# Kernel tuning notes

Measured on AMD Instinct MI355X. Metric: run time of the kernel, lower is better.

Reference implementation:

```python
import jax, jax.numpy as jnp
import numpy as np

DT = 0.01
NJ = 7  # panda: 7 revolute joints, serial chain, fixed base
G_ACC = 9.81


def skew(v):
    x, y, z = v[..., 0], v[..., 1], v[..., 2]
    O = jnp.zeros_like(x)
    return jnp.stack([jnp.stack([O, -z, y], -1),
                      jnp.stack([z, O, -x], -1),
                      jnp.stack([-y, x, O], -1)], -2)


def rodrigues(axis, q):
    # axis [3], q [B] -> [B,3,3]
    K = skew(axis)
    K2 = K @ K
    s = jnp.sin(q)[:, None, None]
    c = jnp.cos(q)[:, None, None]
    return jnp.eye(3, dtype=q.dtype) + s * K + (1.0 - c) * K2


def xmot(E, r, v):
    # motion transform child<-parent; E [B,3,3], r [3], v [B,6] ([w;u] ordering)
    w, u = v[:, :3], v[:, 3:]
    wn = jnp.einsum('bij,bj->bi', E, w)
    un = jnp.einsum('bij,bj->bi', E, u - jnp.cross(jnp.broadcast_to(r, u.shape), w))
    return jnp.concatenate([wn, un], -1)


def crm(v, m):
    # motion cross product v x m
    w, u = v[:, :3], v[:, 3:]
    return jnp.concatenate([jnp.cross(w, m[:, :3]),
                            jnp.cross(w, m[:, 3:]) + jnp.cross(u, m[:, :3])], -1)


def crf(v, f):
    # force cross product v x* f
    w, u = v[:, :3], v[:, 3:]
    n, ff = f[:, :3], f[:, 3:]
    return jnp.concatenate([jnp.cross(w, n) + jnp.cross(u, ff), jnp.cross(w, ff)], -1)


def spatial_inertia(mass, com, inertia):
    # [NJ] / [NJ,3] / [NJ,3,3] -> [NJ,6,6] in [w;v] ordering
    cx = skew(com)
    m = mass[:, None, None]
    top = jnp.concatenate([inertia + m * (cx @ jnp.swapaxes(cx, -1, -2)), m * cx], -1)
    bot = jnp.concatenate([m * jnp.swapaxes(cx, -1, -2),
                           m * jnp.broadcast_to(jnp.eye(3, dtype=mass.dtype), cx.shape)], -1)
    return jnp.concatenate([top, bot], -2)


def aba(q, qd, tau, axes, R_fix, p_fix, mass, com, inertia):
    B = q.shape[0]
    I6 = spatial_inertia(mass, com, inertia)  # [NJ,6,6]
    E_l, S_l, v_l, c_l, IA_l, pA_l = [], [], [], [], [], []
    v_prev = None
    # pass 1: kinematics + bias terms
    for i in range(NJ):
        Rw = jnp.einsum('ij,bjk->bik', R_fix[i], rodrigues(axes[i], q[:, i]))
        E = jnp.swapaxes(Rw, -1, -2)  # parent->child rotation
        S = jnp.concatenate([axes[i], jnp.zeros(3, dtype=q.dtype)])  # [6]
        vJ = qd[:, i:i + 1] * S
        v_i = vJ if i == 0 else xmot(E, p_fix[i], v_prev) + vJ
        c_i = crm(v_i, vJ)
        Iv = jnp.einsum('ij,bj->bi', I6[i], v_i)
        pA_i = crf(v_i, Iv)
        E_l.append(E); S_l.append(S); v_l.append(v_i); c_l.append(c_i)
        IA_l.append(jnp.broadcast_to(I6[i], (B, 6, 6)))
        pA_l.append(pA_i)
        v_prev = v_i
    # pass 2: articulated inertia backward sweep
    U_l = [None] * NJ; d_l = [None] * NJ; uu_l = [None] * NJ
    for i in reversed(range(NJ)):
        S = S_l[i]; IA = IA_l[i]
        U = jnp.einsum('bij,j->bi', IA, S)
        d = jnp.einsum('bi,i->b', U, S)
        uu = tau[:, i] - jnp.einsum('bi,i->b', pA_l[i], S)
        U_l[i], d_l[i], uu_l[i] = U, d, uu
        if i > 0:
            Ia = IA - U[:, :, None] * U[:, None, :] / d[:, None, None]
            pa = pA_l[i] + jnp.einsum('bij,bj->bi', Ia, c_l[i]) + U * (uu / d)[:, None]
            E = E_l[i]; rX = skew(p_fix[i])
            Z = jnp.zeros_like(E)
            Xm = jnp.concatenate([jnp.concatenate([E, Z], -1),
                                  jnp.concatenate([-jnp.einsum('bij,jk->bik', E, rX), E], -1)], -2)
            IA_l[i - 1] = IA_l[i - 1] + jnp.einsum('bji,bjk,bkl->bil', Xm, Ia, Xm)
            fE = jnp.einsum('bji,bj->bi', E, pa[:, 3:])
            nP = jnp.einsum('bji,bj->bi', E, pa[:, :3]) + jnp.cross(jnp.broadcast_to(p_fix[i], fE.shape), fE)
            pA_l[i - 1] = pA_l[i - 1] + jnp.concatenate([nP, fE], -1)
    # pass 3: accelerations (base spatial accel = -gravity)
    a_prev = jnp.broadcast_to(jnp.array([0, 0, 0, 0, 0, G_ACC], dtype=q.dtype), (B, 6))
    qdd = []
    for i in range(NJ):
        ap = xmot(E_l[i], p_fix[i], a_prev) + c_l[i]
        qdd_i = (uu_l[i] - jnp.einsum('bi,bi->b', U_l[i], ap)) / d_l[i]
        a_prev = ap + qdd_i[:, None] * S_l[i]
        qdd.append(qdd_i)
    return jnp.stack(qdd, -1)  # [B,NJ]


def _rx(a):
    c, s = np.cos(a), np.sin(a)
    return np.array([[1, 0, 0], [0, c, -s], [0, s, c]], np.float32)


def setup_inputs() -> dict:
    key = jax.random.key(0)
    k1, k2 = jax.random.split(key)
    B = 262144
    x = 0.5 * jax.random.normal(k1, (B, 2 * NJ), dtype=jnp.float32)
    u = 5.0 * jax.random.normal(k2, (B, NJ), dtype=jnp.float32)
    angles = [0.0, -np.pi / 2, np.pi / 2, np.pi / 2, -np.pi / 2, np.pi / 2, np.pi / 2]
    R_fix = jnp.asarray(np.stack([_rx(a) for a in angles]).astype(np.float32))
    p_fix = jnp.asarray(np.array([[0, 0, 0.333], [0, 0, 0], [0, -0.316, 0], [0.0825, 0, 0],
                                  [-0.0825, 0.384, 0], [0, 0, 0], [0.088, 0, 0]], np.float32))
    axes = jnp.asarray(np.tile(np.array([0, 0, 1], np.float32), (NJ, 1)))
    mass = jnp.asarray(np.array([4.97, 0.65, 3.23, 3.59, 1.23, 1.67, 0.735], np.float32))
    com = jnp.asarray(np.array([[0.003, 0.002, -0.06], [-0.003, -0.028, 0.003], [0.027, 0.039, -0.066],
                                [-0.053, 0.104, 0.027], [-0.012, 0.041, -0.038], [0.06, -0.014, -0.011],
                                [0.01, -0.004, 0.061]], np.float32))
    diags = np.array([[0.7, 0.7, 0.01], [0.008, 0.028, 0.025], [0.037, 0.036, 0.011],
                      [0.026, 0.028, 0.031], [0.036, 0.036, 0.011], [0.002, 0.004, 0.005],
                      [0.012, 0.010, 0.005]], np.float32)
    inertia = jnp.asarray(np.stack([np.diag(v) for v in diags]).astype(np.float32))
    return {"x": x, "u": u, "axes": axes, "R_fix": R_fix, "p_fix": p_fix,
            "mass": mass, "com": com, "inertia": inertia}


def reference(x, u, axes, R_fix, p_fix, mass, com, inertia):
    q, v = x[:, :NJ], x[:, NJ:]
    a = aba(q, v, u, axes, R_fix, p_fix, mass, com, inertia)
    v_next = v + DT * a            # semi-implicit Euler
    q_next = q + DT * v_next
    return jnp.concatenate([q_next, v_next], -1)
```

## Files before the change

kernel.cpp:

```cpp
#include <hip/hip_runtime.h>

#define NJ 7
#define TB 256
static constexpr float DT_C    = 0.01f;
static constexpr float G_ACC_C = 9.81f;

static constexpr float RF[NJ][9] = {
    {1,0,0,  0,1,0,  0,0,1},
    {1,0,0,  0,0,1,  0,-1,0},
    {1,0,0,  0,0,-1, 0,1,0},
    {1,0,0,  0,0,-1, 0,1,0},
    {1,0,0,  0,0,1,  0,-1,0},
    {1,0,0,  0,0,-1, 0,1,0},
    {1,0,0,  0,0,-1, 0,1,0},
};
static constexpr float PFX[NJ][3] = {
    {0.f, 0.f, 0.333f},
    {0.f, 0.f, 0.f},
    {0.f, -0.316f, 0.f},
    {0.0825f, 0.f, 0.f},
    {-0.0825f, 0.384f, 0.f},
    {0.f, 0.f, 0.f},
    {0.088f, 0.f, 0.f},
};
static constexpr float MS[NJ] = {4.97f, 0.65f, 3.23f, 3.59f, 1.23f, 1.67f, 0.735f};
static constexpr float CM[NJ][3] = {
    {0.003f, 0.002f, -0.06f},
    {-0.003f, -0.028f, 0.003f},
    {0.027f, 0.039f, -0.066f},
    {-0.053f, 0.104f, 0.027f},
    {-0.012f, 0.041f, -0.038f},
    {0.06f, -0.014f, -0.011f},
    {0.01f, -0.004f, 0.061f},
};
static constexpr float ID[NJ][3] = {
    {0.7f, 0.7f, 0.01f},
    {0.008f, 0.028f, 0.025f},
    {0.037f, 0.036f, 0.011f},
    {0.026f, 0.028f, 0.031f},
    {0.036f, 0.036f, 0.011f},
    {0.002f, 0.004f, 0.005f},
    {0.012f, 0.01f, 0.005f},
};

struct Derived {
    float J[NJ][6];
    float MC[NJ][3];
};
static constexpr Derived make_derived() {
    Derived d{};
    for (int i = 0; i < NJ; ++i) {
        float m = MS[i], cx = CM[i][0], cy = CM[i][1], cz = CM[i][2];
        float cc = cx*cx + cy*cy + cz*cz;
        d.J[i][0] = ID[i][0] + m*(cc - cx*cx);
        d.J[i][1] = -(m*cx*cy);
        d.J[i][2] = -(m*cx*cz);
        d.J[i][3] = ID[i][1] + m*(cc - cy*cy);
        d.J[i][4] = -(m*cy*cz);
        d.J[i][5] = ID[i][2] + m*(cc - cz*cz);
        d.MC[i][0] = m*cx; d.MC[i][1] = m*cy; d.MC[i][2] = m*cz;
    }
    return d;
}
static constexpr Derived DRV = make_derived();

#define MAKE_E(Rf, s, c)                                                     \
    float E00 = (Rf)[0]*(c) + (Rf)[1]*(s);                                   \
    float E01 = (Rf)[3]*(c) + (Rf)[4]*(s);                                   \
    float E02 = (Rf)[6]*(c) + (Rf)[7]*(s);                                   \
    float E10 = (Rf)[1]*(c) - (Rf)[0]*(s);                                   \
    float E11 = (Rf)[4]*(c) - (Rf)[3]*(s);                                   \
    float E12 = (Rf)[7]*(c) - (Rf)[6]*(s);                                   \
    float E20 = (Rf)[2];                                                     \
    float E21 = (Rf)[5];                                                     \
    float E22 = (Rf)[8];

extern "C" __global__ __launch_bounds__(TB)
void aba_step_kernel(const float* __restrict__ x, const float* __restrict__ u,
                     float* __restrict__ out, int B)
{
    __shared__ float vbuf[TB * 37];

    const int tid = threadIdx.x;
    const int b   = blockIdx.x * TB + tid;
    if (b >= B) return;
    const int xb = b * 14;
    float* vr = vbuf + tid * 37;

    float qr[NJ], qdr[NJ];
    #pragma unroll
    for (int i = 0; i < NJ; ++i) qr[i]  = x[xb + i];
    #pragma unroll
    for (int i = 0; i < NJ; ++i) qdr[i] = x[xb + 7 + i];

    float v0, v1, v2, v3, v4, v5;

    {
        v0 = 0.f; v1 = 0.f; v2 = qdr[0]; v3 = 0.f; v4 = 0.f; v5 = 0.f;
        vr[0] = v0; vr[1] = v1; vr[2] = v2; vr[3] = v3; vr[4] = v4; vr[5] = v5;
        #pragma unroll
        for (int i = 1; i < NJ; ++i) {
            float s, c;
            __sincosf(qr[i], &s, &c);
            MAKE_E(RF[i], s, c)
            const float px = PFX[i][0], py = PFX[i][1], pz = PFX[i][2];
            float t0 = v3 - (py*v2 - pz*v1);
            float t1 = v4 - (pz*v0 - px*v2);
            float t2 = v5 - (px*v1 - py*v0);
            float nw0 = E00*v0 + E01*v1 + E02*v2;
            float nw1 = E10*v0 + E11*v1 + E12*v2;
            float nw2 = E20*v0 + E21*v1 + E22*v2;
            float nu0 = E00*t0 + E01*t1 + E02*t2;
            float nu1 = E10*t0 + E11*t1 + E12*t2;
            float nu2 = E20*t0 + E21*t1 + E22*t2;
            v0 = nw0; v1 = nw1; v2 = nw2 + qdr[i];
            v3 = nu0; v4 = nu1; v5 = nu2;
            if (i < 6) {
                vr[6*i+0] = v0; vr[6*i+1] = v1; vr[6*i+2] = v2;
                vr[6*i+3] = v3; vr[6*i+4] = v4; vr[6*i+5] = v5;
            }
        }
    }

    float PA[6] = {0,0,0,0,0,0};
    float PB[9] = {0,0,0,0,0,0,0,0,0};
    float PC[6] = {0,0,0,0,0,0};
    float AC0=0.f, AC1=0.f, AC2=0.f, AC3=0.f, AC4=0.f, AC5=0.f;
    float u60=0.f, u61=0.f, u62=0.f, u63=0.f, u64=0.f, u65=0.f;

    #pragma unroll 1
    for (int i = 6; i >= 1; --i) {
        const float qd = x[xb + 7 + i];
        const float m   = MS[i];
        const float mcx = DRV.MC[i][0], mcy = DRV.MC[i][1], mcz = DRV.MC[i][2];
        const float J0 = DRV.J[i][0], J1 = DRV.J[i][1], J2 = DRV.J[i][2];
        const float J3 = DRV.J[i][3], J4 = DRV.J[i][4], J5 = DRV.J[i][5];

        float n0 = J0*v0 + J1*v1 + J2*v2 + (mcy*v5 - mcz*v4);
        float n1 = J1*v0 + J3*v1 + J4*v2 + (mcz*v3 - mcx*v5);
        float n2 = J2*v0 + J4*v1 + J5*v2 + (mcx*v4 - mcy*v3);
        float f0 = v1*mcz - v2*mcy + m*v3;
        float f1 = v2*mcx - v0*mcz + m*v4;
        float f2 = v0*mcy - v1*mcx + m*v5;
        float p0 = v1*n2 - v2*n1 + v4*f2 - v5*f1 + AC0;
        float p1 = v2*n0 - v0*n2 + v5*f0 - v3*f2 + AC1;
        float p2 = v0*n1 - v1*n0 + v3*f1 - v4*f0 + AC2;
        float p3 = v1*f2 - v2*f1 + AC3;
        float p4 = v2*f0 - v0*f2 + AC4;
        float p5 = v0*f1 - v1*f0 + AC5;

        float A0 = J0 + PA[0]; float A1 = J1 + PA[1]; float A2 = J2 + PA[2];
        float A3 = J3 + PA[3]; float A4 = J4 + PA[4]; float A5 = J5 + PA[5];
        float B00 = PB[0];        float B01 = PB[1] - mcz;  float B02 = PB[2] + mcy;
        float B10 = PB[3] + mcz;  float B11 = PB[4];        float B12 = PB[5] - mcx;
        float B20 = PB[6] - mcy;  float B21 = PB[7] + mcx;  float B22 = PB[8];
        float C0 = PC[0] + m, C1 = PC[1],     C2 = PC[2];
        float C3 = PC[3] + m, C4 = PC[4],     C5 = PC[5] + m;

        float uu   = u[b*NJ + i] - p2;
        float invd = __builtin_amdgcn_rcpf(A5);
        float k    = uu * invd;
        float t0 = A2*invd, t1 = A4*invd;
        float t3 = B20*invd, t4 = B21*invd, t5 = B22*invd;

        if (i == 6) {
            u60 = t0; u61 = t1; u62 = t3; u63 = t4; u64 = t5; u65 = k;
        } else {
            vr[6*i+0] = t0; vr[6*i+1] = t1; vr[6*i+2] = t3;
            vr[6*i+3] = t4; vr[6*i+4] = t5; vr[6*i+5] = k;
        }

        float a00 = A0 - A2*t0, a01 = A1 - A2*t1, a11 = A3 - A4*t1;
        float b00 = B00 - A2*t3, b01 = B01 - A2*t4, b02 = B02 - A2*t5;
        float b10 = B10 - A4*t3, b11 = B11 - A4*t4, b12 = B12 - A4*t5;
        float c00 = C0 - B20*t3, c01 = C1 - B20*t4, c02 = C2 - B20*t5;
        float c11 = C3 - B21*t4, c12 = C4 - B21*t5, c22 = C5 - B22*t5;

        float q0 = v1*qd, q1 = -v0*qd, q3 = v4*qd, q4 = -v3*qd;
        float pa0 = p0 + a00*q0 + a01*q1 + b00*q3 + b01*q4 + A2*k;
        float pa1 = p1 + a01*q0 + a11*q1 + b10*q3 + b11*q4 + A4*k;
        float pa2 = p2 + uu;
        float pa3 = p3 + b00*q0 + b10*q1 + c00*q3 + c01*q4 + B20*k;
        float pa4 = p4 + b01*q0 + b11*q1 + c01*q3 + c11*q4 + B21*k;
        float pa5 = p5 + b02*q0 + b12*q1 + c02*q3 + c12*q4 + B22*k;

        float s, c;
        __sincosf(x[xb + i], &s, &c);
        const float R0 = RF[i][0], R1 = RF[i][1], R3 = RF[i][3],
                    R4 = RF[i][4], R6 = RF[i][6], R7 = RF[i][7];
        float E00 = R0*c + R1*s, E01 = R3*c + R4*s, E02 = R6*c + R7*s;
        float E10 = R1*c - R0*s, E11 = R4*c - R3*s, E12 = R7*c - R6*s;
        const float E20 = RF[i][2], E21 = RF[i][5], E22 = RF[i][8];
        const float px = PFX[i][0], py = PFX[i][1], pz = PFX[i][2];

        float fE0 = E00*pa3 + E10*pa4 + E20*pa5;
        float fE1 = E01*pa3 + E11*pa4 + E21*pa5;
        float fE2 = E02*pa3 + E12*pa4 + E22*pa5;
        AC0 = E00*pa0 + E10*pa1 + E20*pa2 + (py*fE2 - pz*fE1);
        AC1 = E01*pa0 + E11*pa1 + E21*pa2 + (pz*fE0 - px*fE2);
        AC2 = E02*pa0 + E12*pa1 + E22*pa2 + (px*fE1 - py*fE0);
        AC3 = fE0; AC4 = fE1; AC5 = fE2;

        float AE00 = a00*E00 + a01*E10, AE01 = a00*E01 + a01*E11, AE02 = a00*E02 + a01*E12;
        float AE10 = a01*E00 + a11*E10, AE11 = a01*E01 + a11*E11, AE12 = a01*E02 + a11*E12;
        float Ap00 = E00*AE00 + E10*AE10;
        float Ap01 = E00*AE01 + E10*AE11;
        float Ap02 = E00*AE02 + E10*AE12;
        float Ap11 = E01*AE01 + E11*AE11;
        float Ap12 = E01*AE02 + E11*AE12;
        float Ap22 = E02*AE02 + E12*AE12;
        float BE00 = b00*E00 + b01*E10 + b02*E20;
        float BE01 = b00*E01 + b01*E11 + b02*E21;
        float BE02 = b00*E02 + b01*E12 + b02*E22;
        float BE10 = b10*E00 + b11*E10 + b12*E20;
        float BE11 = b10*E01 + b11*E11 + b12*E21;
        float BE12 = b10*E02 + b11*E12 + b12*E22;
        float Bp00 = E00*BE00 + E10*BE10, Bp01 = E00*BE01 + E10*BE11, Bp02 = E00*BE02 + E10*BE12;
        float Bp10 = E01*BE00 + E11*BE10, Bp11 = E01*BE01 + E11*BE11, Bp12 = E01*BE02 + E11*BE12;
        float Bp20 = E02*BE00 + E12*BE10, Bp21 = E02*BE01 + E12*BE11, Bp22 = E02*BE02 + E12*BE12;
        float CE00 = c00*E00 + c01*E10 + c02*E20;
        float CE01 = c00*E01 + c01*E11 + c02*E21;
        float CE02 = c00*E02 + c01*E12 + c02*E22;
        float CE10 = c01*E00 + c11*E10 + c12*E20;
        float CE11 = c01*E01 + c11*E11 + c12*E21;
        float CE12 = c01*E02 + c11*E12 + c12*E22;
        float CE20 = c02*E00 + c12*E10 + c22*E20;
        float CE21 = c02*E01 + c12*E11 + c22*E21;
        float CE22 = c02*E02 + c12*E12 + c22*E22;
        float Cp00 = E00*CE00 + E10*CE10 + E20*CE20;
        float Cp01 = E00*CE01 + E10*CE11 + E20*CE21;
        float Cp02 = E00*CE02 + E10*CE12 + E20*CE22;
        float Cp11 = E01*CE01 + E11*CE11 + E21*CE21;
        float Cp12 = E01*CE02 + E11*CE12 + E21*CE22;
        float Cp22 = E02*CE02 + E12*CE12 + E22*CE22;
        float G00 = Bp01*pz - Bp02*py, G01 = Bp02*px - Bp00*pz, G02 = Bp00*py - Bp01*px;
        float G10 = Bp11*pz - Bp12*py, G11 = Bp12*px - Bp10*pz, G12 = Bp10*py - Bp11*px;
        float G20 = Bp21*pz - Bp22*py, G21 = Bp22*px - Bp20*pz, G22 = Bp20*py - Bp21*px;
        float H00 = Cp01*pz - Cp02*py, H01 = Cp02*px - Cp00*pz, H02 = Cp00*py - Cp01*px;
        float H10 = Cp11*pz - Cp12*py, H11 = Cp12*px - Cp01*pz, H12 = Cp01*py - Cp11*px;
        float H20 = Cp12*pz - Cp22*py, H21 = Cp22*px - Cp02*pz, H22 = Cp02*py - Cp12*px;
        float PH00 = py*H20 - pz*H10;
        float PH01 = py*H21 - pz*H11;
        float PH02 = py*H22 - pz*H12;
        float PH11 = pz*H01 - px*H21;
        float PH12 = pz*H02 - px*H22;
        float PH22 = px*H12 - py*H02;

        float nv0 = vr[6*(i-1)+0], nv1 = vr[6*(i-1)+1], nv2 = vr[6*(i-1)+2];
        float nv3 = vr[6*(i-1)+3], nv4 = vr[6*(i-1)+4], nv5 = vr[6*(i-1)+5];

        PA[0] = Ap00 - G00 - G00 - PH00;
        PA[1] = Ap01 - G01 - G10 - PH01;
        PA[2] = Ap02 - G02 - G20 - PH02;
        PA[3] = Ap11 - G11 - G11 - PH11;
        PA[4] = Ap12 - G12 - G21 - PH12;
        PA[5] = Ap22 - G22 - G22 - PH22;
        PB[0] = Bp00 + py*Cp02 - pz*Cp01;
        PB[1] = Bp01 + py*Cp12 - pz*Cp11;
        PB[2] = Bp02 + py*Cp22 - pz*Cp12;
        PB[3] = Bp10 + pz*Cp00 - px*Cp02;
        PB[4] = Bp11 + pz*Cp01 - px*Cp12;
        PB[5] = Bp12 + pz*Cp02 - px*Cp22;
        PB[6] = Bp20 + px*Cp01 - py*Cp00;
        PB[7] = Bp21 + px*Cp11 - py*Cp01;
        PB[8] = Bp22 + px*Cp12 - py*Cp02;
        PC[0] = Cp00; PC[1] = Cp01; PC[2] = Cp02;
        PC[3] = Cp11; PC[4] = Cp12; PC[5] = Cp22;

        v0 = nv0; v1 = nv1; v2 = nv2; v3 = nv3; v4 = nv4; v5 = nv5;
    }

    {
        const float m   = MS[0];
        const float mcx = DRV.MC[0][0], mcy = DRV.MC[0][1], mcz = DRV.MC[0][2];
        const float J0 = DRV.J[0][0], J1 = DRV.J[0][1], J2 = DRV.J[0][2];
        const float J3 = DRV.J[0][3], J4 = DRV.J[0][4], J5 = DRV.J[0][5];
        float n0 = J0*v0 + J1*v1 + J2*v2 + (mcy*v5 - mcz*v4);
        float n1 = J1*v0 + J3*v1 + J4*v2 + (mcz*v3 - mcx*v5);
        float n2 = J2*v0 + J4*v1 + J5*v2 + (mcx*v4 - mcy*v3);
        float f0 = v1*mcz - v2*mcy + m*v3;
        float f1 = v2*mcx - v0*mcz + m*v4;
        float f2 = v0*mcy - v1*mcx + m*v5;
        float p2 = v0*n1 - v1*n0 + v3*f1 - v4*f0 + AC2;
        float A2 = J2 + PA[2];
        float A4 = J4 + PA[4];
        float A5 = J5 + PA[5];
        float B20 = PB[6] - mcy;  float B21 = PB[7] + mcx;  float B22 = PB[8];
        float uu   = u[b*NJ + 0] - p2;
        float invd = __builtin_amdgcn_rcpf(A5);
        float k    = uu * invd;
        vr[0] = A2*invd; vr[1] = A4*invd; vr[2] = B20*invd;
        vr[3] = B21*invd; vr[4] = B22*invd; vr[5] = k;
        (void)n2; (void)f2;
    }

    {
        float a0=0.f, a1=0.f, a2=0.f, a3=0.f, a4=0.f, a5=G_ACC_C;
        float w0=0.f, w1=0.f, w2=0.f, w3=0.f, w4=0.f, w5=0.f;
        #pragma unroll
        for (int i = 0; i < NJ; ++i) {
            const float qd = qdr[i];
            float s, c;
            __sincosf(qr[i], &s, &c);
            MAKE_E(RF[i], s, c)
            const float px = PFX[i][0], py = PFX[i][1], pz = PFX[i][2];
            if (i == 0) {
                w2 = qd;
            } else {
                float r0 = w3 - (py*w2 - pz*w1);
                float r1 = w4 - (pz*w0 - px*w2);
                float r2 = w5 - (px*w1 - py*w0);
                float nw0 = E00*w0 + E01*w1 + E02*w2;
                float nw1 = E10*w0 + E11*w1 + E12*w2;
                float nw2 = E20*w0 + E21*w1 + E22*w2;
                float nu0 = E00*r0 + E01*r1 + E02*r2;
                float nu1 = E10*r0 + E11*r1 + E12*r2;
                float nu2 = E20*r0 + E21*r1 + E22*r2;
                w0 = nw0; w1 = nw1; w2 = nw2 + qd;
                w3 = nu0; w4 = nu1; w5 = nu2;
            }
            float cl0 = w1*qd, cl1 = -w0*qd, cl3 = w4*qd, cl4 = -w3*qd;
            float r0 = a3 - (py*a2 - pz*a1);
            float r1 = a4 - (pz*a0 - px*a2);
            float r2 = a5 - (px*a1 - py*a0);
            float ap0 = E00*a0 + E01*a1 + E02*a2 + cl0;
            float ap1 = E10*a0 + E11*a1 + E12*a2 + cl1;
            float ap2 = E20*a0 + E21*a1 + E22*a2;
            float ap3 = E00*r0 + E01*r1 + E02*r2 + cl3;
            float ap4 = E10*r0 + E11*r1 + E12*r2 + cl4;
            float ap5 = E20*r0 + E21*r1 + E22*r2;
            float d0, d1, d2, d3, d4, d5;
            if (i == 6) {
                d0 = u60; d1 = u61; d2 = u62; d3 = u63; d4 = u64; d5 = u65;
            } else {
                d0 = vr[6*i+0]; d1 = vr[6*i+1]; d2 = vr[6*i+2];
                d3 = vr[6*i+3]; d4 = vr[6*i+4]; d5 = vr[6*i+5];
            }
            float qdd = d5 - (d0*ap0 + d1*ap1 + ap2 + d2*ap3 + d3*ap4 + d4*ap5);
            a0 = ap0; a1 = ap1; a2 = ap2 + qdd;
            a3 = ap3; a4 = ap4; a5 = ap5;
            float vn = qd + DT_C*qdd;
            out[xb + 7 + i] = vn;
            out[xb + i]     = qr[i] + DT_C*vn;
        }
    }
}

extern "C" void kernel_launch(void* const* d_in, const int* in_sizes, int n_in,
                              void* d_out, int out_size, void* d_ws, size_t ws_size,
                              hipStream_t stream) {
    const float* x = (const float*)d_in[0];
    const float* u = (const float*)d_in[1];
    float* out = (float*)d_out;
    int B = in_sizes[0] / (2*NJ);
    int threads = TB;
    int blocks = (B + threads - 1) / threads;
    hipLaunchKernelGGL(aba_step_kernel, dim3(blocks), dim3(threads), 0, stream,
                       x, u, out, B);
}
```

Before: 108.1 us.

## Process two batch elements per thread with interleaved independent dependency chains

Each thread now handles two robots, sample t and sample t+B/2, and the forward, backward and final passes interleave the work of both. The goal is more instruction-level parallelism, so the long serial ABA dependency chains can hide each other's latency. The block size is halved to keep shared memory per block the same. In exchange, register pressure roughly doubles, which may cut occupancy or cause spills. Joint angles and rates are now reloaded from global memory instead of being cached in registers.

Result: slower. 118.2 us (+9.3%).

```diff
diff --git a/kernel.cpp b/kernel.cpp
--- a/kernel.cpp
+++ b/kernel.cpp
@@ -1,7 +1,7 @@
 #include <hip/hip_runtime.h>
 
 #define NJ 7
-#define TB 256
+#define TB 128
 static constexpr float DT_C    = 0.01f;
 static constexpr float G_ACC_C = 9.81f;
 
@@ -79,31 +79,39 @@
 void aba_step_kernel(const float* __restrict__ x, const float* __restrict__ u,
                      float* __restrict__ out, int B)
 {
-    __shared__ float vbuf[TB * 37];
-
-    const int tid = threadIdx.x;
-    const int b   = blockIdx.x * TB + tid;
-    if (b >= B) return;
-    const int xb = b * 14;
-    float* vr = vbuf + tid * 37;
-
-    float qr[NJ], qdr[NJ];
+    __shared__ float vbuf[2 * TB * 37];
+
+    const int tid    = threadIdx.x;
+    const int halfUp = (B + 1) >> 1;
+    const int t      = blockIdx.x * TB + tid;
+    if (t >= halfUp) return;
+    int b1 = t + halfUp;
+    if (b1 >= B) b1 = t;
+    const int bb[2] = { t, b1 };
+    const int xb[2] = { bb[0] * 14, bb[1] * 14 };
+    float* const vr[2] = { vbuf + tid * 37, vbuf + (TB + tid) * 37 };
+
+    float v[2][6];
+
     #pragma unroll
-    for (int i = 0; i < NJ; ++i) qr[i]  = x[xb + i];
+    for (int it = 0; it < 2; ++it) {
+        float qd0 = x[xb[it] + 7];
+        v[it][0]=0.f; v[it][1]=0.f; v[it][2]=qd0;
+        v[it][3]=0.f; v[it][4]=0.f; v[it][5]=0.f;
+        vr[it][0]=0.f; vr[it][1]=0.f; vr[it][2]=qd0;
+        vr[it][3]=0.f; vr[it][4]=0.f; vr[it][5]=0.f;
+    }
     #pragma unroll
-    for (int i = 0; i < NJ; ++i) qdr[i] = x[xb + 7 + i];
-
-    float v0, v1, v2, v3, v4, v5;
-
-    {
-        v0 = 0.f; v1 = 0.f; v2 = qdr[0]; v3 = 0.f; v4 = 0.f; v5 = 0.f;
-        vr[0] = v0; vr[1] = v1; vr[2] = v2; vr[3] = v3; vr[4] = v4; vr[5] = v5;
+    for (int i = 1; i < NJ; ++i) {
         #pragma unroll
-        for (int i = 1; i < NJ; ++i) {
+        for (int it = 0; it < 2; ++it) {
             float s, c;
-            __sincosf(qr[i], &s, &c);
+            __sincosf(x[xb[it] + i], &s, &c);
             MAKE_E(RF[i], s, c)
             const float px = PFX[i][0], py = PFX[i][1], pz = PFX[i][2];
+            const float qd = x[xb[it] + 7 + i];
+            float v0=v[it][0], v1=v[it][1], v2=v[it][2];
+            float v3=v[it][3], v4=v[it][4], v5=v[it][5];
             float t0 = v3 - (py*v2 - pz*v1);
             float t1 = v4 - (pz*v0 - px*v2);
             float t2 = v5 - (px*v1 - py*v0);
@@ -113,235 +121,263 @@
             float nu0 = E00*t0 + E01*t1 + E02*t2;
             float nu1 = E10*t0 + E11*t1 + E12*t2;
             float nu2 = E20*t0 + E21*t1 + E22*t2;
-            v0 = nw0; v1 = nw1; v2 = nw2 + qdr[i];
-            v3 = nu0; v4 = nu1; v5 = nu2;
+            v[it][0]=nw0; v[it][1]=nw1; v[it][2]=nw2+qd;
+            v[it][3]=nu0; v[it][4]=nu1; v[it][5]=nu2;
             if (i < 6) {
-                vr[6*i+0] = v0; vr[6*i+1] = v1; vr[6*i+2] = v2;
-                vr[6*i+3] = v3; vr[6*i+4] = v4; vr[6*i+5] = v5;
+                vr[it][6*i+0]=v[it][0]; vr[it][6*i+1]=v[it][1]; vr[it][6*i+2]=v[it][2];
+                vr[it][6*i+3]=v[it][3]; vr[it][6*i+4]=v[it][4]; vr[it][6*i+5]=v[it][5];
             }
         }
     }
 
-    float PA[6] = {0,0,0,0,0,0};
-    float PB[9] = {0,0,0,0,0,0,0,0,0};
-    float PC[6] = {0,0,0,0,0,0};
-    float AC0=0.f, AC1=0.f, AC2=0.f, AC3=0.f, AC4=0.f, AC5=0.f;
-    float u60=0.f, u61=0.f, u62=0.f, u63=0.f, u64=0.f, u65=0.f;
+    float PAa[2][6] = {{0,0,0,0,0,0},{0,0,0,0,0,0}};
+    float PBa[2][9] = {{0,0,0,0,0,0,0,0,0},{0,0,0,0,0,0,0,0,0}};
+    float PCa[2][6] = {{0,0,0,0,0,0},{0,0,0,0,0,0}};
+    float ACa[2][6] = {{0,0,0,0,0,0},{0,0,0,0,0,0}};
+    float U6[2][6];
 
     #pragma unroll 1
     for (int i = 6; i >= 1; --i) {
-        const float qd = x[xb + 7 + i];
         const float m   = MS[i];
         const float mcx = DRV.MC[i][0], mcy = DRV.MC[i][1], mcz = DRV.MC[i][2];
         const float J0 = DRV.J[i][0], J1 = DRV.J[i][1], J2 = DRV.J[i][2];
         const float J3 = DRV.J[i][3], J4 = DRV.J[i][4], J5 = DRV.J[i][5];
-
-        float n0 = J0*v0 + J1*v1 + J2*v2 + (mcy*v5 - mcz*v4);
-        float n1 = J1*v0 + J3*v1 + J4*v2 + (mcz*v3 - mcx*v5);
-        float n2 = J2*v0 + J4*v1 + J5*v2 + (mcx*v4 - mcy*v3);
-        float f0 = v1*mcz - v2*mcy + m*v3;
-        float f1 = v2*mcx - v0*mcz + m*v4;
-        float f2 = v0*mcy - v1*mcx + m*v5;
-        float p0 = v1*n2 - v2*n1 + v4*f2 - v5*f1 + AC0;
-        float p1 = v2*n0 - v0*n2 + v5*f0 - v3*f2 + AC1;
-        float p2 = v0*n1 - v1*n0 + v3*f1 - v4*f0 + AC2;
-        float p3 = v1*f2 - v2*f1 + AC3;
-        float p4 = v2*f0 - v0*f2 + AC4;
-        float p5 = v0*f1 - v1*f0 + AC5;
-
-        float A0 = J0 + PA[0]; float A1 = J1 + PA[1]; float A2 = J2 + PA[2];
-        float A3 = J3 + PA[3]; float A4 = J4 + PA[4]; float A5 = J5 + PA[5];
-        float B00 = PB[0];        float B01 = PB[1] - mcz;  float B02 = PB[2] + mcy;
-        float B10 = PB[3] + mcz;  float B11 = PB[4];        float B12 = PB[5] - mcx;
-        float B20 = PB[6] - mcy;  float B21 = PB[7] + mcx;  float B22 = PB[8];
-        float C0 = PC[0] + m, C1 = PC[1],     C2 = PC[2];
-        float C3 = PC[3] + m, C4 = PC[4],     C5 = PC[5] + m;
-
-        float uu   = u[b*NJ + i] - p2;
-        float invd = __builtin_amdgcn_rcpf(A5);
-        float k    = uu * invd;
-        float t0 = A2*invd, t1 = A4*invd;
-        float t3 = B20*invd, t4 = B21*invd, t5 = B22*invd;
-
-        if (i == 6) {
-            u60 = t0; u61 = t1; u62 = t3; u63 = t4; u64 = t5; u65 = k;
-        } else {
-            vr[6*i+0] = t0; vr[6*i+1] = t1; vr[6*i+2] = t3;
-            vr[6*i+3] = t4; vr[6*i+4] = t5; vr[6*i+5] = k;
-        }
-
-        float a00 = A0 - A2*t0, a01 = A1 - A2*t1, a11 = A3 - A4*t1;
-        float b00 = B00 - A2*t3, b01 = B01 - A2*t4, b02 = B02 - A2*t5;
-        float b10 = B10 - A4*t3, b11 = B11 - A4*t4, b12 = B12 - A4*t5;
-        float c00 = C0 - B20*t3, c01 = C1 - B20*t4, c02 = C2 - B20*t5;
-        float c11 = C3 - B21*t4, c12 = C4 - B21*t5, c22 = C5 - B22*t5;
-
-        float q0 = v1*qd, q1 = -v0*qd, q3 = v4*qd, q4 = -v3*qd;
-        float pa0 = p0 + a00*q0 + a01*q1 + b00*q3 + b01*q4 + A2*k;
-        float pa1 = p1 + a01*q0 + a11*q1 + b10*q3 + b11*q4 + A4*k;
-        float pa2 = p2 + uu;
-        float pa3 = p3 + b00*q0 + b10*q1 + c00*q3 + c01*q4 + B20*k;
-        float pa4 = p4 + b01*q0 + b11*q1 + c01*q3 + c11*q4 + B21*k;
-        float pa5 = p5 + b02*q0 + b12*q1 + c02*q3 + c12*q4 + B22*k;
-
-        float s, c;
-        __sincosf(x[xb + i], &s, &c);
         const float R0 = RF[i][0], R1 = RF[i][1], R3 = RF[i][3],
                     R4 = RF[i][4], R6 = RF[i][6], R7 = RF[i][7];
-        float E00 = R0*c + R1*s, E01 = R3*c + R4*s, E02 = R6*c + R7*s;
-        float E10 = R1*c - R0*s, E11 = R4*c - R3*s, E12 = R7*c - R6*s;
-        const float E20 = RF[i][2], E21 = RF[i][5], E22 = RF[i][8];
+        const float E20c = RF[i][2], E21c = RF[i][5], E22c = RF[i][8];
         const float px = PFX[i][0], py = PFX[i][1], pz = PFX[i][2];
 
-        float fE0 = E00*pa3 + E10*pa4 + E20*pa5;
-        float fE1 = E01*pa3 + E11*pa4 + E21*pa5;
-        float fE2 = E02*pa3 + E12*pa4 + E22*pa5;
-        AC0 = E00*pa0 + E10*pa1 + E20*pa2 + (py*fE2 - pz*fE1);
-        AC1 = E01*pa0 + E11*pa1 + E21*pa2 + (pz*fE0 - px*fE2);
-        AC2 = E02*pa0 + E12*pa1 + E22*pa2 + (px*fE1 - py*fE0);
-        AC3 = fE0; AC4 = fE1; AC5 = fE2;
-
-        float AE00 = a00*E00 + a01*E10, AE01 = a00*E01 + a01*E11, AE02 = a00*E02 + a01*E12;
-        float AE10 = a01*E00 + a11*E10, AE11 = a01*E01 + a11*E11, AE12 = a01*E02 + a11*E12;
-        float Ap00 = E00*AE00 + E10*AE10;
-        float Ap01 = E00*AE01 + E10*AE11;
-        float Ap02 = E00*AE02 + E10*AE12;
-        float Ap11 = E01*AE01 + E11*AE11;
-        float Ap12 = E01*AE02 + E11*AE12;
-        float Ap22 = E02*AE02 + E12*AE12;
-        float BE00 = b00*E00 + b01*E10 + b02*E20;
-        float BE01 = b00*E01 + b01*E11 + b02*E21;
-        float BE02 = b00*E02 + b01*E12 + b02*E22;
-        float BE10 = b10*E00 + b11*E10 + b12*E20;
-        float BE11 = b10*E01 + b11*E11 + b12*E21;
-        float BE12 = b10*E02 + b11*E12 + b12*E22;
-        float Bp00 = E00*BE00 + E10*BE10, Bp01 = E00*BE01 + E10*BE11, Bp02 = E00*BE02 + E10*BE12;
-        float Bp10 = E01*BE00 + E11*BE10, Bp11 = E01*BE01 + E11*BE11, Bp12 = E01*BE02 + E11*BE12;
-        float Bp20 = E02*BE00 + E12*BE10, Bp21 = E02*BE01 + E12*BE11, Bp22 = E02*BE02 + E12*BE12;
-        float CE00 = c00*E00 + c01*E10 + c02*E20;
-        float CE01 = c00*E01 + c01*E11 + c02*E21;
-        float CE02 = c00*E02 + c01*E12 + c02*E22;
-        float CE10 = c01*E00 + c11*E10 + c12*E20;
-        float CE11 = c01*E01 + c11*E11 + c12*E21;
-        float CE12 = c01*E02 + c11*E12 + c12*E22;
-        float CE20 = c02*E00 + c12*E10 + c22*E20;
-        float CE21 = c02*E01 + c12*E11 + c22*E21;
-        float CE22 = c02*E02 + c12*E12 + c22*E22;
-        float Cp00 = E00*CE00 + E10*CE10 + E20*CE20;
-        float Cp01 = E00*CE01 + E10*CE11 + E20*CE21;
-        float Cp02 = E00*CE02 + E10*CE12 + E20*CE22;
-        float Cp11 = E01*CE01 + E11*CE11 + E21*CE21;
-        float Cp12 = E01*CE02 + E11*CE12 + E21*CE22;
-        float Cp22 = E02*CE02 + E12*CE12 + E22*CE22;
-        float G00 = Bp01*pz - Bp02*py, G01 = Bp02*px - Bp00*pz, G02 = Bp00*py - Bp01*px;
-        float G10 = Bp11*pz - Bp12*py, G11 = Bp12*px - Bp10*pz, G12 = Bp10*py - Bp11*px;
-        float G20 = Bp21*pz - Bp22*py, G21 = Bp22*px - Bp20*pz, G22 = Bp20*py - Bp21*px;
-        float H00 = Cp01*pz - Cp02*py, H01 = Cp02*px - Cp00*pz, H02 = Cp00*py - Cp01*px;
-        float H10 = Cp11*pz - Cp12*py, H11 = Cp12*px - Cp01*pz, H12 = Cp01*py - Cp11*px;
-        float H20 = Cp12*pz - Cp22*py, H21 = Cp22*px - Cp02*pz, H22 = Cp02*py - Cp12*px;
-        float PH00 = py*H20 - pz*H10;
-        float PH01 = py*H21 - pz*H11;
-        float PH02 = py*H22 - pz*H12;
-        float PH11 = pz*H01 - px*H21;
-        float PH12 = pz*H02 - px*H22;
-        float PH22 = px*H12 - py*H02;
-
-        float nv0 = vr[6*(i-1)+0], nv1 = vr[6*(i-1)+1], nv2 = vr[6*(i-1)+2];
-        float nv3 = vr[6*(i-1)+3], nv4 = vr[6*(i-1)+4], nv5 = vr[6*(i-1)+5];
-
-        PA[0] = Ap00 - G00 - G00 - PH00;
-        PA[1] = Ap01 - G01 - G10 - PH01;
-        PA[2] = Ap02 - G02 - G20 - PH02;
-        PA[3] = Ap11 - G11 - G11 - PH11;
-        PA[4] = Ap12 - G12 - G21 - PH12;
-        PA[5] = Ap22 - G22 - G22 - PH22;
-        PB[0] = Bp00 + py*Cp02 - pz*Cp01;
-        PB[1] = Bp01 + py*Cp12 - pz*Cp11;
-        PB[2] = Bp02 + py*Cp22 - pz*Cp12;
-        PB[3] = Bp10 + pz*Cp00 - px*Cp02;
-        PB[4] = Bp11 + pz*Cp01 - px*Cp12;
-        PB[5] = Bp12 + pz*Cp02 - px*Cp22;
-        PB[6] = Bp20 + px*Cp01 - py*Cp00;
-        PB[7] = Bp21 + px*Cp11 - py*Cp01;
-        PB[8] = Bp22 + px*Cp12 - py*Cp02;
-        PC[0] = Cp00; PC[1] = Cp01; PC[2] = Cp02;
-        PC[3] = Cp11; PC[4] = Cp12; PC[5] = Cp22;
-
-        v0 = nv0; v1 = nv1; v2 = nv2; v3 = nv3; v4 = nv4; v5 = nv5;
-    }
-
-    {
+        #pragma unroll
+        for (int it = 0; it < 2; ++it) {
+            const float qd  = x[xb[it] + 7 + i];
+            const float tau = u[bb[it]*NJ + i];
+            float s, c;
+            __sincosf(x[xb[it] + i], &s, &c);
+
+            const float v0=v[it][0], v1=v[it][1], v2=v[it][2];
+            const float v3=v[it][3], v4=v[it][4], v5=v[it][5];
+
+            float n0 = J0*v0 + J1*v1 + J2*v2 + (mcy*v5 - mcz*v4);
+            float n1 = J1*v0 + J3*v1 + J4*v2 + (mcz*v3 - mcx*v5);
+            float n2 = J2*v0 + J4*v1 + J5*v2 + (mcx*v4 - mcy*v3);
+            float f0 = v1*mcz - v2*mcy + m*v3;
+            float f1 = v2*mcx - v0*mcz + m*v4;
+            float f2 = v0*mcy - v1*mcx + m*v5;
+            float p0 = v1*n2 - v2*n1 + v4*f2 - v5*f1 + ACa[it][0];
+            float p1 = v2*n0 - v0*n2 + v5*f0 - v3*f2 + ACa[it][1];
+            float p2 = v0*n1 - v1*n0 + v3*f1 - v4*f0 + ACa[it][2];
+            float p3 = v1*f2 - v2*f1 + ACa[it][3];
+            float p4 = v2*f0 - v0*f2 + ACa[it][4];
+            float p5 = v0*f1 - v1*f0 + ACa[it][5];
+
+            float A0 = J0 + PAa[it][0]; float A1 = J1 + PAa[it][1]; float A2 = J2 + PAa[it][2];
+            float A3 = J3 + PAa[it][3]; float A4 = J4 + PAa[it][4]; float A5 = J5 + PAa[it][5];
+            float B00 = PBa[it][0];        float B01 = PBa[it][1] - mcz;  float B02 = PBa[it][2] + mcy;
+            float B10 = PBa[it][3] + mcz;  float B11 = PBa[it][4];        float B12 = PBa[it][5] - mcx;
+            float B20 = PBa[it][6] - mcy;  float B21 = PBa[it][7] + mcx;  float B22 = PBa[it][8];
+            float C0 = PCa[it][0] + m, C1 = PCa[it][1],     C2 = PCa[it][2];
+            float C3 = PCa[it][3] + m, C4 = PCa[it][4],     C5 = PCa[it][5] + m;
+
+            float uu   = tau - p2;
+            float invd = __builtin_amdgcn_rcpf(A5);
+            float k    = uu * invd;
+            float t0 = A2*invd, t1 = A4*invd;
+            float t3 = B20*invd, t4 = B21*invd, t5 = B22*invd;
+
+            if (i == 6) {
+                U6[it][0]=t0; U6[it][1]=t1; U6[it][2]=t3;
+                U6[it][3]=t4; U6[it][4]=t5; U6[it][5]=k;
+            } else {
+                vr[it][6*i+0]=t0; vr[it][6*i+1]=t1; vr[it][6*i+2]=t3;
+                vr[it][6*i+3]=t4; vr[it][6*i+4]=t5; vr[it][6*i+5]=k;
+            }
+
+            float a00 = A0 - A2*t0, a01 = A1 - A2*t1, a11 = A3 - A4*t1;
+            float b00 = B00 - A2*t3, b01 = B01 - A2*t4, b02 = B02 - A2*t5;
+            float b10 = B10 - A4*t3, b11 = B11 - A4*t4, b12 = B12 - A4*t5;
+            float c00 = C0 - B20*t3, c01 = C1 - B20*t4, c02 = C2 - B20*t5;
+            float c11 = C3 - B21*t4, c12 = C4 - B21*t5, c22 = C5 - B22*t5;
+
+            float q0 = v1*qd, q1 = -v0*qd, q3 = v4*qd, q4 = -v3*qd;
+            float pa0 = p0 + a00*q0 + a01*q1 + b00*q3 + b01*q4 + A2*k;
+            float pa1 = p1 + a01*q0 + a11*q1 + b10*q3 + b11*q4 + A4*k;
+            float pa2 = p2 + uu;
+            float pa3 = p3 + b00*q0 + b10*q1 + c00*q3 + c01*q4 + B20*k;
+            float pa4 = p4 + b01*q0 + b11*q1 + c01*q3 + c11*q4 + B21*k;
+            float pa5 = p5 + b02*q0 + b12*q1 + c02*q3 + c12*q4 + B22*k;
+
+            float E00 = R0*c + R1*s, E01 = R3*c + R4*s, E02 = R6*c + R7*s;
+            float E10 = R1*c - R0*s, E11 = R4*c - R3*s, E12 = R7*c - R6*s;
+            const float E20 = E20c, E21 = E21c, E22 = E22c;
+
+            float fE0 = E00*pa3 + E10*pa4 + E20*pa5;
+            float fE1 = E01*pa3 + E11*pa4 + E21*pa5;
+            float fE2 = E02*pa3 + E12*pa4 + E22*pa5;
+            ACa[it][0] = E00*pa0 + E10*pa1 + E20*pa2 + (py*fE2 - pz*fE1);
+            ACa[it][1] = E01*pa0 + E11*pa1 + E21*pa2 + (pz*fE0 - px*fE2);
+            ACa[it][2] = E02*pa0 + E12*pa1 + E22*pa2 + (px*fE1 - py*fE0);
+            ACa[it][3] = fE0; ACa[it][4] = fE1; ACa[it][5] = fE2;
+
+            float AE00 = a00*E00 + a01*E10, AE01 = a00*E01 + a01*E11, AE02 = a00*E02 + a01*E12;
+            float AE10 = a01*E00 + a11*E10, AE11 = a01*E01 + a11*E11, AE12 = a01*E02 + a11*E12;
+            float Ap00 = E00*AE00 + E10*AE10;
+            float Ap01 = E00*AE01 + E10*AE11;
+            float Ap02 = E00*AE02 + E10*AE12;
+            float Ap11 = E01*AE01 + E11*AE11;
+            float Ap12 = E01*AE02 + E11*AE12;
+            float Ap22 = E02*AE02 + E12*AE12;
+            float BE00 = b00*E00 + b01*E10 + b02*E20;
+            float BE01 = b00*E01 + b01*E11 + b02*E21;
+            float BE02 = b00*E02 + b01*E12 + b02*E22;
+            float BE10 = b10*E00 + b11*E10 + b12*E20;
+            float BE11 = b10*E01 + b11*E11 + b12*E21;
+            float BE12 = b10*E02 + b11*E12 + b12*E22;
+            float Bp00 = E00*BE00 + E10*BE10, Bp01 = E00*BE01 + E10*BE11, Bp02 = E00*BE02 + E10*BE12;
+            float Bp10 = E01*BE00 + E11*BE10, Bp11 = E01*BE01 + E11*BE11, Bp12 = E01*BE02 + E11*BE12;
+            float Bp20 = E02*BE00 + E12*BE10, Bp21 = E02*BE01 + E12*BE11, Bp22 = E02*BE02 + E12*BE12;
+            float CE00 = c00*E00 + c01*E10 + c02*E20;
+            float CE01 = c00*E01 + c01*E11 + c02*E21;
+            float CE02 = c00*E02 + c01*E12 + c02*E22;
+            float CE10 = c01*E00 + c11*E10 + c12*E20;
+            float CE11 = c01*E01 + c11*E11 + c12*E21;
+            float CE12 = c01*E02 + c11*E12 + c12*E22;
+            float CE20 = c02*E00 + c12*E10 + c22*E20;
+            float CE21 = c02*E01 + c12*E11 + c22*E21;
+            float CE22 = c02*E02 + c12*E12 + c22*E22;
+            float Cp00 = E00*CE00 + E10*CE10 + E20*CE20;
+            float Cp01 = E00*CE01 + E10*CE11 + E20*CE21;
+            float Cp02 = E00*CE02 + E10*CE12 + E20*CE22;
+            float Cp11 = E01*CE01 + E11*CE11 + E21*CE21;
+            float Cp12 = E01*CE02 + E11*CE12 + E21*CE22;
+            float Cp22 = E02*CE02 + E12*CE12 + E22*CE22;
+            float G00 = Bp01*pz - Bp02*py, G01 = Bp02*px - Bp00*pz, G02 = Bp00*py - Bp01*px;
+            float G10 = Bp11*pz - Bp12*py, G11 = Bp12*px - Bp10*pz, G12 = Bp10*py - Bp11*px;
+            float G20 = Bp21*pz - Bp22*py, G21 = Bp22*px - Bp20*pz, G22 = Bp20*py - Bp21*px;
+            float H00 = Cp01*pz - Cp02*py, H01 = Cp02*px - Cp00*pz, H02 = Cp00*py - Cp01*px;
+            float H10 = Cp11*pz - Cp12*py, H11 = Cp12*px - Cp01*pz, H12 = Cp01*py - Cp11*px;
+            float H20 = Cp12*pz - Cp22*py, H21 = Cp22*px - Cp02*pz, H22 = Cp02*py - Cp12*px;
+            float PH00 = py*H20 - pz*H10;
+            float PH01 = py*H21 - pz*H11;
+            float PH02 = py*H22 - pz*H12;
+            float PH11 = pz*H01 - px*H21;
+            float PH12 = pz*H02 - px*H22;
+            float PH22 = px*H12 - py*H02;
+
+            float nv0 = vr[it][6*(i-1)+0], nv1 = vr[it][6*(i-1)+1], nv2 = vr[it][6*(i-1)+2];
+            float nv3 = vr[it][6*(i-1)+3], nv4 = vr[it][6*(i-1)+4], nv5 = vr[it][6*(i-1)+5];
+
+            PAa[it][0] = Ap00 - G00 - G00 - PH00;
+            PAa[it][1] = Ap01 - G01 - G10 - PH01;
+            PAa[it][2] = Ap02 - G02 - G20 - PH02;
+            PAa[it][3] = Ap11 - G11 - G11 - PH11;
+            PAa[it][4] = Ap12 - G12 - G21 - PH12;
+            PAa[it][5] = Ap22 - G22 - G22 - PH22;
+            PBa[it][0] = Bp00 + py*Cp02 - pz*Cp01;
+            PBa[it][1] = Bp01 + py*Cp12 - pz*Cp11;
+            PBa[it][2] = Bp02 + py*Cp22 - pz*Cp12;
+            PBa[it][3] = Bp10 + pz*Cp00 - px*Cp02;
+            PBa[it][4] = Bp11 + pz*Cp01 - px*Cp12;
+            PBa[it][5] = Bp12 + pz*Cp02 - px*Cp22;
+            PBa[it][6] = Bp20 + px*Cp01 - py*Cp00;
+            PBa[it][7] = Bp21 + px*Cp11 - py*Cp01;
+            PBa[it][8] = Bp22 + px*Cp12 - py*Cp02;
+            PCa[it][0] = Cp00; PCa[it][1] = Cp01; PCa[it][2] = Cp02;
+            PCa[it][3] = Cp11; PCa[it][4] = Cp12; PCa[it][5] = Cp22;
+
+            v[it][0]=nv0; v[it][1]=nv1; v[it][2]=nv2;
+            v[it][3]=nv3; v[it][4]=nv4; v[it][5]=nv5;
+        }
+    }
+
+    #pragma unroll
+    for (int it = 0; it < 2; ++it) {
         const float m   = MS[0];
         const float mcx = DRV.MC[0][0], mcy = DRV.MC[0][1], mcz = DRV.MC[0][2];
         const float J0 = DRV.J[0][0], J1 = DRV.J[0][1], J2 = DRV.J[0][2];
         const float J3 = DRV.J[0][3], J4 = DRV.J[0][4], J5 = DRV.J[0][5];
+        const float v0=v[it][0], v1=v[it][1], v2=v[it][2];
+        const float v3=v[it][3], v4=v[it][4], v5=v[it][5];
         float n0 = J0*v0 + J1*v1 + J2*v2 + (mcy*v5 - mcz*v4);
         float n1 = J1*v0 + J3*v1 + J4*v2 + (mcz*v3 - mcx*v5);
-        float n2 = J2*v0 + J4*v1 + J5*v2 + (mcx*v4 - mcy*v3);
         float f0 = v1*mcz - v2*mcy + m*v3;
         float f1 = v2*mcx - v0*mcz + m*v4;
-        float f2 = v0*mcy - v1*mcx + m*v5;
-        float p2 = v0*n1 - v1*n0 + v3*f1 - v4*f0 + AC2;
-        float A2 = J2 + PA[2];
-        float A4 = J4 + PA[4];
-        float A5 = J5 + PA[5];
-        float B20 = PB[6] - mcy;  float B21 = PB[7] + mcx;  float B22 = PB[8];
-        float uu   = u[b*NJ + 0] - p2;
+        float p2 = v0*n1 - v1*n0 + v3*f1 - v4*f0 + ACa[it][2];
+        float A2 = J2 + PAa[it][2];
+        float A4 = J4 + PAa[it][4];
+        float A5 = J5 + PAa[it][5];
+        float B20 = PBa[it][6] - mcy;  float B21 = PBa[it][7] + mcx;  float B22 = PBa[it][8];
+        float uu   = u[bb[it]*NJ + 0] - p2;
         float invd = __builtin_amdgcn_rcpf(A5);
         float k    = uu * invd;
-        vr[0] = A2*invd; vr[1] = A4*invd; vr[2] = B20*invd;
-        vr[3] = B21*invd; vr[4] = B22*invd; vr[5] = k;
-        (void)n2; (void)f2;
+        vr[it][0] = A2*invd;  vr[it][1] = A4*invd; vr[it][2] = B20*invd;
+        vr[it][3] = B21*invd; vr[it][4] = B22*invd; vr[it][5] = k;
     }
 
     {
-        float a0=0.f, a1=0.f, a2=0.f, a3=0.f, a4=0.f, a5=G_ACC_C;
-        float w0=0.f, w1=0.f, w2=0.f, w3=0.f, w4=0.f, w5=0.f;
+        float aa[2][6], ww[2][6];
+        #pragma unroll
+        for (int it = 0; it < 2; ++it) {
+            aa[it][0]=0.f; aa[it][1]=0.f; aa[it][2]=0.f;
+            aa[it][3]=0.f; aa[it][4]=0.f; aa[it][5]=G_ACC_C;
+            ww[it][0]=0.f; ww[it][1]=0.f; ww[it][2]=0.f;
+            ww[it][3]=0.f; ww[it][4]=0.f; ww[it][5]=0.f;
+        }
         #pragma unroll
         for (int i = 0; i < NJ; ++i) {
-            const float qd = qdr[i];
-            float s, c;
-            __sincosf(qr[i], &s, &c);
-            MAKE_E(RF[i], s, c)
-            const float px = PFX[i][0], py = PFX[i][1], pz = PFX[i][2];
-            if (i == 0) {
-                w2 = qd;
-            } else {
-                float r0 = w3 - (py*w2 - pz*w1);
-                float r1 = w4 - (pz*w0 - px*w2);
-                float r2 = w5 - (px*w1 - py*w0);
-                float nw0 = E00*w0 + E01*w1 + E02*w2;
-                float nw1 = E10*w0 + E11*w1 + E12*w2;
-                float nw2 = E20*w0 + E21*w1 + E22*w2;
-                float nu0 = E00*r0 + E01*r1 + E02*r2;
-                float nu1 = E10*r0 + E11*r1 + E12*r2;
-                float nu2 = E20*r0 + E21*r1 + E22*r2;
-                w0 = nw0; w1 = nw1; w2 = nw2 + qd;
-                w3 = nu0; w4 = nu1; w5 = nu2;
+            #pragma unroll
+            for (int it = 0; it < 2; ++it) {
+                const float qi = x[xb[it] + i];
+                const float qd = x[xb[it] + 7 + i];
+                float s, c;
+                __sincosf(qi, &s, &c);
+                MAKE_E(RF[i], s, c)
+                const float px = PFX[i][0], py = PFX[i][1], pz = PFX[i][2];
+                float w0=ww[it][0], w1=ww[it][1], w2=ww[it][2];
+                float w3=ww[it][3], w4=ww[it][4], w5=ww[it][5];
+                if (i == 0) {
+                    w2 = qd;
+                } else {
+                    float r0 = w3 - (py*w2 - pz*w1);
+                    float r1 = w4 - (pz*w0 - px*w2);
+                    float r2 = w5 - (px*w1 - py*w0);
+                    float nw0 = E00*w0 + E01*w1 + E02*w2;
+                    float nw1 = E10*w0 + E11*w1 + E12*w2;
+                    float nw2 = E20*w0 + E21*w1 + E22*w2;
+                    float nu0 = E00*r0 + E01*r1 + E02*r2;
+                    float nu1 = E10*r0 + E11*r1 + E12*r2;
+                    float nu2 = E20*r0 + E21*r1 + E22*r2;
+                    w0 = nw0; w1 = nw1; w2 = nw2 + qd;
+                    w3 = nu0; w4 = nu1; w5 = nu2;
+                }
+                ww[it][0]=w0; ww[it][1]=w1; ww[it][2]=w2;
+                ww[it][3]=w3; ww[it][4]=w4; ww[it][5]=w5;
+                float cl0 = w1*qd, cl1 = -w0*qd, cl3 = w4*qd, cl4 = -w3*qd;
+                float a0=aa[it][0], a1=aa[it][1], a2=aa[it][2];
+                float a3=aa[it][3], a4=aa[it][4], a5=aa[it][5];
+                float r0 = a3 - (py*a2 - pz*a1);
+                float r1 = a4 - (pz*a0 - px*a2);
+                float r2 = a5 - (px*a1 - py*a0);
+                float ap0 = E00*a0 + E01*a1 + E02*a2 + cl0;
+                float ap1 = E10*a0 + E11*a1 + E12*a2 + cl1;
+                float ap2 = E20*a0 + E21*a1 + E22*a2;
+                float ap3 = E00*r0 + E01*r1 + E02*r2 + cl3;
+                float ap4 = E10*r0 + E11*r1 + E12*r2 + cl4;
+                float ap5 = E20*r0 + E21*r1 + E22*r2;
+                float d0, d1, d2, d3, d4, d5;
+                if (i == 6) {
+                    d0=U6[it][0]; d1=U6[it][1]; d2=U6[it][2];
+                    d3=U6[it][3]; d4=U6[it][4]; d5=U6[it][5];
+                } else {
+                    d0=vr[it][6*i+0]; d1=vr[it][6*i+1]; d2=vr[it][6*i+2];
+                    d3=vr[it][6*i+3]; d4=vr[it][6*i+4]; d5=vr[it][6*i+5];
+                }
+                float qdd = d5 - (d0*ap0 + d1*ap1 + ap2 + d2*ap3 + d3*ap4 + d4*ap5);
+                aa[it][0]=ap0; aa[it][1]=ap1; aa[it][2]=ap2+qdd;
+                aa[it][3]=ap3; aa[it][4]=ap4; aa[it][5]=ap5;
+                float vn = qd + DT_C*qdd;
+                out[xb[it] + 7 + i] = vn;
+                out[xb[it] + i]     = qi + DT_C*vn;
             }
-            float cl0 = w1*qd, cl1 = -w0*qd, cl3 = w4*qd, cl4 = -w3*qd;
-            float r0 = a3 - (py*a2 - pz*a1);
-            float r1 = a4 - (pz*a0 - px*a2);
-            float r2 = a5 - (px*a1 - py*a0);
-            float ap0 = E00*a0 + E01*a1 + E02*a2 + cl0;
-            float ap1 = E10*a0 + E11*a1 + E12*a2 + cl1;
-            float ap2 = E20*a0 + E21*a1 + E22*a2;
-            float ap3 = E00*r0 + E01*r1 + E02*r2 + cl3;
-            float ap4 = E10*r0 + E11*r1 + E12*r2 + cl4;
-            float ap5 = E20*r0 + E21*r1 + E22*r2;
-            float d0, d1, d2, d3, d4, d5;
-            if (i == 6) {
-                d0 = u60; d1 = u61; d2 = u62; d3 = u63; d4 = u64; d5 = u65;
-            } else {
-                d0 = vr[6*i+0]; d1 = vr[6*i+1]; d2 = vr[6*i+2];
-                d3 = vr[6*i+3]; d4 = vr[6*i+4]; d5 = vr[6*i+5];
-            }
-            float qdd = d5 - (d0*ap0 + d1*ap1 + ap2 + d2*ap3 + d3*ap4 + d4*ap5);
-            a0 = ap0; a1 = ap1; a2 = ap2 + qdd;
-            a3 = ap3; a4 = ap4; a5 = ap5;
-            float vn = qd + DT_C*qdd;
-            out[xb + 7 + i] = vn;
-            out[xb + i]     = qr[i] + DT_C*vn;
         }
     }
 }
@@ -353,8 +389,9 @@
     const float* u = (const float*)d_in[1];
     float* out = (float*)d_out;
     int B = in_sizes[0] / (2*NJ);
+    int halfUp = (B + 1) >> 1;
     int threads = TB;
-    int blocks = (B + threads - 1) / threads;
+    int blocks = (halfUp + threads - 1) / threads;
     hipLaunchKernelGGL(aba_step_kernel, dim3(blocks), dim3(threads), 0, stream,
                        x, u, out, B);
 }
```
